# Performance work log

Hardware: AMD Instinct MI355X
Metric: run time of the kernel (lower is better)

Reference implementation:

```python
import jax, jax.numpy as jnp
import numpy as np

# ---- problem dims (match init_kwargs / input_specs) ----
MC = 2048        # max_concepts
D = 128          # embed_dim
B = 64           # batch
L = 16           # program length
NOBJ = 128       # objects per scene
FDIM = 512       # feature_dim
NN = MC + NOBJ   # num_nodes
TEMP = 3.0       # cosine temperature
TH = 0.8         # true_th (cosine, train==val)
POS = 10.0
NEG = -10.0
YES_IDX = 0      # protocol['concepts','yes']
NO_IDX = 1       # protocol['concepts','no']
INIT_VAR = 0.001


def setup_inputs() -> dict:
    key = jax.random.key(0)
    ks = jax.random.split(key, 6)
    scene = jax.random.normal(ks[0], (B, NOBJ, FDIM), jnp.float32)
    # program[:, :, 0] = op code in [0,7), program[:, :, 1] = argument index
    program = jax.random.randint(ks[1], (B, L, 2), 0, 7, dtype=jnp.int32)
    concept_table = jax.random.normal(ks[2], (MC, D), jnp.float32) * INIT_VAR
    relation_table = jax.random.normal(ks[3], (MC, D * D), jnp.float32) * INIT_VAR
    W_feat = jax.random.normal(ks[4], (FDIM, D), jnp.float32) * INIT_VAR
    b_feat = jax.random.normal(ks[5], (D,), jnp.float32) * INIT_VAR
    return {"scene": scene, "program": program, "concept_table": concept_table,
            "relation_table": relation_table, "W_feat": W_feat, "b_feat": b_feat}


def _cos_sim(x, y, eps=1e-8):
    # torch F.cosine_similarity semantics: clamp each norm at eps
    xn = jnp.maximum(jnp.linalg.norm(x, axis=-1), eps)
    yn = jnp.maximum(jnp.linalg.norm(y, axis=-1), eps)
    return jnp.sum(x * y, axis=-1) / (xn * yn)


def reference(scene, program, concept_table, relation_table, W_feat, b_feat):
    # feature_mlp (dim_hidden == 0 -> single Linear)
    objects = scene @ W_feat + b_feat                              # [B, NOBJ, D]
    # per-step embedded arguments
    concept_args = concept_table[program[:, :, 1]]                 # [B, L, D]
    rel_args = relation_table[program[:, :, 1]].reshape(B, L, D, D)
    node_is_concept = jnp.arange(NN) < MC                          # [NN]
    # all_nodes = concat(all_concepts, objects) per sample
    all_nodes = jnp.concatenate(
        [jnp.broadcast_to(concept_table[None], (B, MC, D)), objects], axis=1)  # [B, NN, D]

    def run_sample(nodes_i, ops_i, args_i, cargs_i, rargs_i):
        att0 = jnp.ones((NN,), jnp.float32)

        def body(att, inp):
            op, arg, cvec, rmat = inp

            def f_null(a):
                return a

            def f_sel_obj(a):  # select 'object_only': zero concept slots
                return jnp.where(node_is_concept, 0.0, a)

            def f_sel_con(a):  # select 'concept_only': zero object slots
                return jnp.where(node_is_concept, a, 0.0)

            def f_verify(a):
                sim = _cos_sim(nodes_i, cvec[None, :])             # [NN]
                return jnp.minimum(a, jax.nn.sigmoid((sim - TH) * TEMP))

            def f_choose(a):
                a = jnp.where(node_is_concept, 0.0, a)
                return a.at[arg].set(1.0)

            def f_exist(a):
                s = a.max()
                yes = s * POS
                no = POS - yes
                a = jnp.full_like(a, NEG)
                return a.at[YES_IDX].set(yes).at[NO_IDX].set(no)

            def f_transfer(a):
                gather = a @ nodes_i                               # [D]
                trans = gather @ rmat                              # [D]
                sim = _cos_sim(nodes_i, trans[None, :])            # [NN]
                return jax.nn.sigmoid((sim - TH) * TEMP) * a.max()

            new = jax.lax.switch(
                op, [f_null, f_sel_obj, f_sel_con, f_verify, f_choose,
                     f_exist, f_transfer], att)
            return new, new

        _, hist = jax.lax.scan(body, att0, (ops_i, args_i, cargs_i, rargs_i))
        return hist                                                # [L, NN]

    hist = jax.vmap(run_sample)(all_nodes, program[:, :, 0], program[:, :, 1],
                                concept_args, rel_args)            # [B, L, NN]
    attn_final = hist[:, -1, :MC]                                  # [B, MC]
    out = jax.nn.log_softmax(attn_final, axis=1)
    return out, hist
```

## Files before the change

kernel.cpp:

```cpp
#include <hip/hip_runtime.h>
#include <math.h>

#define MC   2048
#define DD   128
#define BB   64
#define LL   16
#define NOBJ 128
#define FDIM 512
#define NN   (MC + NOBJ)
#define TEMPC 3.0f
#define THC   0.8f
#define POSC  10.0f
#define NEGC  (-10.0f)
#define EPSC  1e-8f
#define NARG  8
#define NINF  (-3.402823466e38f)
#define NSCALE 256.0f

#define QB   4
#define PART (NN / QB)
#define TS   512

typedef unsigned short ushort_t;
typedef float v2f __attribute__((ext_vector_type(2)));

#if defined(__has_builtin)
#if __has_builtin(__builtin_amdgcn_cvt_pk_f32_fp8)
#define HAS_HW_FP8 1
#endif
#endif

__device__ __forceinline__ float e4m3_dec1(unsigned int bv) {
    unsigned int s = (bv >> 7) & 1u, E = (bv >> 3) & 15u, M = bv & 7u;
    float v;
    if (E) v = __uint_as_float(((E + 120u) << 23) | (M << 20));
    else   v = (float)M * 0.001953125f;
    return s ? -v : v;
}
__device__ __forceinline__ v2f f8pair_sw(unsigned int w) {
    v2f r; r[0] = e4m3_dec1(w & 0xffu); r[1] = e4m3_dec1((w >> 8) & 0xffu); return r;
}
#ifdef HAS_HW_FP8
#define F8LO(u) __builtin_amdgcn_cvt_pk_f32_fp8((u), false)
#define F8HI(u) __builtin_amdgcn_cvt_pk_f32_fp8((u), true)
#else
#define F8LO(u) f8pair_sw((u) & 0xffffu)
#define F8HI(u) f8pair_sw((u) >> 16)
#endif

__device__ __forceinline__ unsigned int f32_to_e4m3(float x) {
    float a = fabsf(x);
    unsigned int s = (__float_as_uint(x) >> 31) << 7;
    if (a == 0.0f) return s;
    if (a >= 448.0f) return s | 0x7Eu;
    int e; float m = frexpf(a, &e);
    if (e >= -5) {
        int mant = (int)rintf(m * 16.0f);
        if (mant == 16) { mant = 8; e++; if (e - 1 > 8) return s | 0x7Eu; }
        return s | ((unsigned)(e - 1 + 7) << 3) | (unsigned)(mant - 8);
    } else {
        int q = (int)rintf(a * 512.0f);
        if (q >= 8) return s | 0x08u;
        return s | (unsigned)q;
    }
}

#define DEC16(u, g) do { \
    v2f _p0 = F8LO((u).x), _p1 = F8HI((u).x), _p2 = F8LO((u).y), _p3 = F8HI((u).y); \
    v2f _p4 = F8LO((u).z), _p5 = F8HI((u).z), _p6 = F8LO((u).w), _p7 = F8HI((u).w); \
    g[0]=_p0[0]; g[1]=_p0[1]; g[2]=_p1[0];  g[3]=_p1[1]; \
    g[4]=_p2[0]; g[5]=_p2[1]; g[6]=_p3[0];  g[7]=_p3[1]; \
    g[8]=_p4[0]; g[9]=_p4[1]; g[10]=_p5[0]; g[11]=_p5[1]; \
    g[12]=_p6[0]; g[13]=_p6[1]; g[14]=_p7[0]; g[15]=_p7[1]; \
} while (0)

__global__ __launch_bounds__(256) void gemm_objects(
        const float* __restrict__ scene, const float* __restrict__ W,
        const float* __restrict__ bias, float* __restrict__ obj) {
    __shared__ float sA[64][68];
    __shared__ float sB[64][68];
    const int b  = blockIdx.y;
    const int mt = (blockIdx.x >> 1) * 64;
    const int nt = (blockIdx.x & 1) * 64;
    const int tid = threadIdx.x;
    const int tx = tid & 15, ty = tid >> 4;
    float acc[4][4] = {{0.f,0.f,0.f,0.f},{0.f,0.f,0.f,0.f},{0.f,0.f,0.f,0.f},{0.f,0.f,0.f,0.f}};
    const float* sc = scene + (size_t)b * NOBJ * FDIM;
    for (int k0 = 0; k0 < FDIM; k0 += 64) {
        {
            const int o  = tid >> 2;
            const int ks = (tid & 3) * 16;
            const float4* src = (const float4*)(sc + (size_t)(mt + o) * FDIM + k0 + ks);
            #pragma unroll
            for (int j4 = 0; j4 < 4; j4++) {
                float4 v = src[j4];
                sA[ks + j4*4 + 0][o] = v.x;
                sA[ks + j4*4 + 1][o] = v.y;
                sA[ks + j4*4 + 2][o] = v.z;
                sA[ks + j4*4 + 3][o] = v.w;
            }
        }
        {
            const int kk = tid >> 2;
            const int dq = (tid & 3) * 16;
            const float4* src = (const float4*)(W + (size_t)(k0 + kk) * DD + nt + dq);
            float4* dst = (float4*)&sB[kk][dq];
            #pragma unroll
            for (int j4 = 0; j4 < 4; j4++) dst[j4] = src[j4];
        }
        __syncthreads();
        #pragma unroll 8
        for (int kk = 0; kk < 64; kk++) {
            float4 a4 = *(const float4*)&sA[kk][ty * 4];
            float4 b4 = *(const float4*)&sB[kk][tx * 4];
            float av[4] = {a4.x, a4.y, a4.z, a4.w};
            float bv[4] = {b4.x, b4.y, b4.z, b4.w};
            #pragma unroll
            for (int i = 0; i < 4; i++)
                #pragma unroll
                for (int j = 0; j < 4; j++)
                    acc[i][j] = fmaf(av[i], bv[j], acc[i][j]);
        }
        __syncthreads();
    }
    #pragma unroll
    for (int i = 0; i < 4; i++) {
        const int o = mt + ty * 4 + i;
        float4 r;
        r.x = acc[i][0] + bias[nt + tx*4 + 0];
        r.y = acc[i][1] + bias[nt + tx*4 + 1];
        r.z = acc[i][2] + bias[nt + tx*4 + 2];
        r.w = acc[i][3] + bias[nt + tx*4 + 3];
        *(float4*)(obj + ((size_t)b * NOBJ + o) * DD + nt + tx*4) = r;
    }
}

__global__ __launch_bounds__(256) void norms_prep(
        const float* __restrict__ ct, const float* __restrict__ obj,
        float* __restrict__ cnorm, float* __restrict__ onorm,
        unsigned char* __restrict__ ctf8, unsigned char* __restrict__ objf8,
        unsigned int* __restrict__ ctr) {
    if (blockIdx.x == 0) {
        for (int i = threadIdx.x; i < BB * 16; i += 256) ctr[i] = 0u;
    }
    const int wid = threadIdx.x >> 6, lane = threadIdx.x & 63;
    const int r = blockIdx.x * 4 + wid;
    const int NROWS = MC + BB * NOBJ;
    if (r >= NROWS) return;
    const float* row = (r < MC) ? (ct + (size_t)r * DD) : (obj + (size_t)(r - MC) * DD);
    unsigned char* brow = (r < MC) ? (ctf8 + (size_t)r * DD) : (objf8 + (size_t)(r - MC) * DD);
    float2 xy = *(const float2*)(row + lane * 2);
    float ss = xy.x * xy.x + xy.y * xy.y;
    #pragma unroll
    for (int off = 32; off; off >>= 1) ss += __shfl_xor(ss, off, 64);
    float nrm = fmaxf(sqrtf(ss), EPSC);
    float inv = NSCALE / nrm;
    unsigned int b0 = f32_to_e4m3(xy.x * inv);
    unsigned int b1 = f32_to_e4m3(xy.y * inv);
    *(ushort_t*)(brow + lane * 2) = (ushort_t)(b0 | (b1 << 8));
    if (lane == 0) {
        if (r < MC) cnorm[r] = nrm;
        else        onorm[r - MC] = nrm;
    }
}

__global__ __launch_bounds__(256) void sig_table(
        const float* __restrict__ ct, const float* __restrict__ obj,
        const float* __restrict__ cnorm, const float* __restrict__ onorm,
        float* __restrict__ sigc, float* __restrict__ sigo) {
    __shared__ float cv[NARG][DD];
    __shared__ float cn[NARG];
    const int tid = threadIdx.x;
    for (int a = 0; a < NARG; a++)
        for (int i = tid; i < DD; i += 256) cv[a][i] = ct[(size_t)a * DD + i];
    if (tid < NARG) cn[tid] = fmaxf(cnorm[tid], EPSC);
    __syncthreads();
    const int sub = tid & 7, slot = tid >> 3;
    #pragma unroll
    for (int p = 0; p < 2; p++) {
        const int r = blockIdx.x * 64 + p * 32 + slot;
        const float* row = (r < MC) ? (ct + (size_t)r * DD) : (obj + (size_t)(r - MC) * DD);
        float4 r0 = *(const float4*)(row + sub * 16 + 0);
        float4 r1 = *(const float4*)(row + sub * 16 + 4);
        float4 r2 = *(const float4*)(row + sub * 16 + 8);
        float4 r3 = *(const float4*)(row + sub * 16 + 12);
        float rn = fmaxf((r < MC) ? cnorm[r] : onorm[r - MC], EPSC);
        for (int a = 0; a < NARG; a++) {
            const float* c = &cv[a][sub * 16];
            float dp = 0.f;
            dp = fmaf(r0.x, c[0], dp);  dp = fmaf(r0.y, c[1], dp);
            dp = fmaf(r0.z, c[2], dp);  dp = fmaf(r0.w, c[3], dp);
            dp = fmaf(r1.x, c[4], dp);  dp = fmaf(r1.y, c[5], dp);
            dp = fmaf(r1.z, c[6], dp);  dp = fmaf(r1.w, c[7], dp);
            dp = fmaf(r2.x, c[8], dp);  dp = fmaf(r2.y, c[9], dp);
            dp = fmaf(r2.z, c[10], dp); dp = fmaf(r2.w, c[11], dp);
            dp = fmaf(r3.x, c[12], dp); dp = fmaf(r3.y, c[13], dp);
            dp = fmaf(r3.z, c[14], dp); dp = fmaf(r3.w, c[15], dp);
            dp += __shfl_xor(dp, 1, 64);
            dp += __shfl_xor(dp, 2, 64);
            dp += __shfl_xor(dp, 4, 64);
            if (sub == 0) {
                float sim = dp / (rn * cn[a]);
                float g = 1.f / (1.f + __expf(-(sim - THC) * TEMPC));
                if (r < MC) sigc[(size_t)a * MC + r] = g;
                else {
                    int ro = r - MC, bb = ro >> 7, oo = ro & 127;
                    sigo[((size_t)bb * NARG + a) * NOBJ + oo] = g;
                }
            }
        }
    }
}


#define GATH_ROW(row_) do { \
    const int _r = (row_); \
    uint4 _u = *(const uint4*)&nd[_r * DD + ((sub ^ (_r & 7)) << 4)]; \
    const float _a = att[_r] * nrmL[_r]; \
    float _g[16]; DEC16(_u, _g); \
    _Pragma("unroll") \
    for (int _j = 0; _j < 16; _j++) ac[_j] = fmaf(_a, _g[_j], ac[_j]); \
} while (0)

#define SIM_ROW(row_, COMB) do { \
    const int _r = (row_); \
    uint4 _u = *(const uint4*)&nd[_r * DD + ((sub ^ (_r & 7)) << 4)]; \
    float _g[16]; DEC16(_u, _g); \
    float _dp = 0.f; \
    _Pragma("unroll") \
    for (int _j = 0; _j < 16; _j++) _dp = fmaf(_g[_j], vv[_j], _dp); \
    _dp += __shfl_xor(_dp, 1, 64); \
    _dp += __shfl_xor(_dp, 2, 64); \
    _dp += __shfl_xor(_dp, 4, 64); \
    if (sub == 0) { \
        const float _sim = _dp * invden; \
        const float sg = 1.f / (1.f + __expf(-(_sim - THC) * TEMPC)); \
        COMB; \
    } \
} while (0)

#define QBARRIER() do { \
    __syncthreads(); \
    if (tid == 0) { \
        __threadfence(); \
        __hip_atomic_fetch_add(myctr, 1u, __ATOMIC_RELEASE, __HIP_MEMORY_SCOPE_AGENT); \
        const unsigned _tgt = (unsigned)(QB * epoch); \
        while (__hip_atomic_load(myctr, __ATOMIC_ACQUIRE, __HIP_MEMORY_SCOPE_AGENT) < _tgt) {} \
    } \
    __syncthreads(); \
} while (0)

__global__ __launch_bounds__(TS) void scan_exec(
        const float* __restrict__ ct, const float* __restrict__ rt,
        const int* __restrict__ program,
        const float* __restrict__ cnorm, const float* __restrict__ onorm,
        const float* __restrict__ sigc, const float* __restrict__ sigo,
        const unsigned char* __restrict__ ctf8, const unsigned char* __restrict__ objf8,
        float* __restrict__ gpart, unsigned int* __restrict__ ctr,
        float* __restrict__ out, float* __restrict__ hist) {

    const int b    = blockIdx.x & (BB - 1);
    const int q    = blockIdx.x >> 6;
    const int base = q * PART;
    const int tid  = threadIdx.x;
    const int lane = tid & 63, wid = tid >> 6;
    const int rg   = tid >> 3, sub = tid & 7;

    __shared__ __align__(16) unsigned char nd[PART * DD];
    __shared__ __align__(16) float att[PART];
    __shared__ __align__(16) float nrmL[PART];
    __shared__ __align__(16) float vec[DD];
    __shared__ __align__(16) float gvf[DD];
    __shared__ __align__(16) float part[8 * DD];
    __shared__ float wred[8];
    __shared__ float red2[8];
    __shared__ float s_sh;
    __shared__ int   sprog[2 * LL];

    const unsigned char* myobjf8 = objf8 + (size_t)b * NOBJ * DD;

    for (int idx = tid; idx < PART * 8; idx += TS) {
        const int row = idx >> 3, j = idx & 7;
        const int g   = base + row;
        const unsigned char* src = (g < MC) ? (ctf8 + (size_t)g * DD)
                                            : (myobjf8 + (size_t)(g - MC) * DD);
        uint4 v = *(const uint4*)(src + j * 16);
        *(uint4*)&nd[row * DD + ((j ^ (row & 7)) << 4)] = v;
    }
    for (int i = tid; i < PART; i += TS) {
        const int g = base + i;
        att[i]  = 1.0f;
        nrmL[i] = (g < MC) ? cnorm[g] : onorm[b * NOBJ + (g - MC)];
    }
    if (tid < 2 * LL) sprog[tid] = program[b * 2 * LL + tid];
    __syncthreads();

    unsigned int epoch = 0;
    float* gpb = gpart + (size_t)b * (2 * QB * 132);
    unsigned int* myctr = ctr + b * 16;

    for (int step = 0; step < LL; step++) {
        const int op  = sprog[2 * step];
        const int arg = sprog[2 * step + 1];
        float* hrow = hist + ((size_t)b * LL + step) * NN;

        if (op == 0) {
            for (int i = tid; i < PART; i += TS) hrow[base + i] = att[i];
        } else if (op == 1) {
            for (int i = tid; i < PART; i += TS) {
                const int g = base + i;
                const float nv = (g < MC) ? 0.0f : att[i];
                att[i] = nv; hrow[g] = nv;
            }
        } else if (op == 2) {
            for (int i = tid; i < PART; i += TS) {
                const int g = base + i;
                const float nv = (g < MC) ? att[i] : 0.0f;
                att[i] = nv; hrow[g] = nv;
            }
        } else if (op == 3 && arg < NARG) {
            const float* sc = sigc + (size_t)arg * MC;
            const float* so = sigo + ((size_t)b * NARG + arg) * NOBJ;
            for (int i = tid; i < PART; i += TS) {
                const int g = base + i;
                const float gg = (g < MC) ? sc[g] : so[g - MC];
                const float nv = fminf(att[i], gg);
                att[i] = nv; hrow[g] = nv;
            }
        } else if (op == 3) {
            __syncthreads();
            if (tid < DD) vec[tid] = ct[(size_t)arg * DD + tid];
            __syncthreads();
            const float cn = fmaxf(cnorm[arg], EPSC);
            const float invden = 1.0f / (NSCALE * cn);
            float vv[16];
            {
                const float4 v0 = *(const float4*)&vec[sub * 16 + 0];
                const float4 v1 = *(const float4*)&vec[sub * 16 + 4];
                const float4 v2 = *(const float4*)&vec[sub * 16 + 8];
                const float4 v3 = *(const float4*)&vec[sub * 16 + 12];
                vv[0]=v0.x; vv[1]=v0.y; vv[2]=v0.z; vv[3]=v0.w;
                vv[4]=v1.x; vv[5]=v1.y; vv[6]=v1.z; vv[7]=v1.w;
                vv[8]=v2.x; vv[9]=v2.y; vv[10]=v2.z; vv[11]=v2.w;
                vv[12]=v3.x; vv[13]=v3.y; vv[14]=v3.z; vv[15]=v3.w;
            }
            #pragma unroll
            for (int p = 0; p < 8; p++) SIM_ROW(rg + p * 64, att[_r] = fminf(att[_r], sg));
            if (rg < PART - 512) SIM_ROW(rg + 512, att[_r] = fminf(att[_r], sg));
            __syncthreads();
            for (int i = tid; i < PART; i += TS) hrow[base + i] = att[i];
        } else if (op == 4) {
            for (int i = tid; i < PART; i += TS) {
                const int g = base + i;
                const float nv = (g < MC) ? ((g == arg) ? 1.0f : 0.0f) : att[i];
                att[i] = nv; hrow[g] = nv;
            }
        } else if (op == 5) {
            __syncthreads();
            float lm = NINF;
            for (int i = tid; i < PART; i += TS) lm = fmaxf(lm, att[i]);
            #pragma unroll
            for (int off = 32; off; off >>= 1) lm = fmaxf(lm, __shfl_xor(lm, off, 64));
            if (lane == 0) wred[wid] = lm;
            __syncthreads();
            epoch++;
            if (tid == 0) {
                float m = wred[0];
                #pragma unroll
                for (int w = 1; w < 8; w++) m = fmaxf(m, wred[w]);
                __hip_atomic_store(&gpb[(size_t)((epoch & 1) * QB + q) * 132 + DD], m,
                                   __ATOMIC_RELAXED, __HIP_MEMORY_SCOPE_AGENT);
            }
            QBARRIER();
            if (tid == 0) {
                float* slotR = gpb + (size_t)((epoch & 1) * QB) * 132;
                float m = NINF;
                #pragma unroll
                for (int k = 0; k < QB; k++)
                    m = fmaxf(m, __hip_atomic_load(&slotR[k * 132 + DD],
                                 __ATOMIC_RELAXED, __HIP_MEMORY_SCOPE_AGENT));
                s_sh = m;
            }
            __syncthreads();
            const float s = s_sh;
            const float yes = s * POSC, no = POSC - yes;
            for (int i = tid; i < PART; i += TS) {
                const int g = base + i;
                const float nv = (g == 0) ? yes : ((g == 1) ? no : NEGC);
                att[i] = nv; hrow[g] = nv;
            }
        } else if (op == 6) {
            __syncthreads();
            float lm = NINF;
            for (int i = tid; i < PART; i += TS) lm = fmaxf(lm, att[i]);
            #pragma unroll
            for (int off = 32; off; off >>= 1) lm = fmaxf(lm, __shfl_xor(lm, off, 64));
            if (lane == 0) wred[wid] = lm;
            float ac[16];
            #pragma unroll
            for (int j = 0; j < 16; j++) ac[j] = 0.f;
            #pragma unroll
            for (int p = 0; p < 8; p++) GATH_ROW(rg + p * 64);
            if (rg < PART - 512) GATH_ROW(rg + 512);
            #pragma unroll
            for (int j = 0; j < 16; j++) {
                ac[j] += __shfl_xor(ac[j], 8, 64);
                ac[j] += __shfl_xor(ac[j], 16, 64);
                ac[j] += __shfl_xor(ac[j], 32, 64);
            }
            if (lane < 8) {
                float* dst = &part[wid * DD + lane * 16];
                #pragma unroll
                for (int k = 0; k < 4; k++)
                    *(float4*)(dst + k * 4) = make_float4(ac[k*4], ac[k*4+1], ac[k*4+2], ac[k*4+3]);
            }
            __syncthreads();
            epoch++;
            {
                float* slotW = gpb + (size_t)((epoch & 1) * QB + q) * 132;
                if (tid < DD) {
                    float gsum = 0.f;
                    #pragma unroll
                    for (int w = 0; w < 8; w++) gsum += part[w * DD + tid];
                    __hip_atomic_store(&slotW[tid], gsum, __ATOMIC_RELAXED, __HIP_MEMORY_SCOPE_AGENT);
                }
                if (tid == DD) {
                    float m = wred[0];
                    #pragma unroll
                    for (int w = 1; w < 8; w++) m = fmaxf(m, wred[w]);
                    __hip_atomic_store(&slotW[DD], m, __ATOMIC_RELAXED, __HIP_MEMORY_SCOPE_AGENT);
                }
            }
            const float* rm = rt + (size_t)arg * (DD * DD);
            const int half = lane >> 5, dq = (lane & 31) * 4;
            float4 rmr[8];
            #pragma unroll
            for (int j = 0; j < 8; j++) {
                const int d = wid * 16 + half * 8 + j;
                rmr[j] = *(const float4*)(rm + (size_t)d * DD + dq);
            }
            QBARRIER();
            {
                float* slotR = gpb + (size_t)((epoch & 1) * QB) * 132;
                if (tid < DD) {
                    float gsum = 0.f;
                    #pragma unroll
                    for (int k = 0; k < QB; k++)
                        gsum += __hip_atomic_load(&slotR[k * 132 + tid],
                                  __ATOMIC_RELAXED, __HIP_MEMORY_SCOPE_AGENT);
                    gvf[tid] = gsum;
                }
                if (tid == DD) {
                    float m = NINF;
                    #pragma unroll
                    for (int k = 0; k < QB; k++)
                        m = fmaxf(m, __hip_atomic_load(&slotR[k * 132 + DD],
                                     __ATOMIC_RELAXED, __HIP_MEMORY_SCOPE_AGENT));
                    s_sh = m;
                }
            }
            __syncthreads();
            float qx = 0.f, qy = 0.f, qz = 0.f, qw = 0.f;
            #pragma unroll
            for (int j = 0; j < 8; j++) {
                const int d = wid * 16 + half * 8 + j;
                const float g = gvf[d];
                qx = fmaf(g, rmr[j].x, qx); qy = fmaf(g, rmr[j].y, qy);
                qz = fmaf(g, rmr[j].z, qz); qw = fmaf(g, rmr[j].w, qw);
            }
            qx += __shfl_xor(qx, 32, 64); qy += __shfl_xor(qy, 32, 64);
            qz += __shfl_xor(qz, 32, 64); qw += __shfl_xor(qw, 32, 64);
            if (lane < 32) *(float4*)&part[wid * DD + dq] = make_float4(qx, qy, qz, qw);
            __syncthreads();
            if (tid < DD) {
                float t = 0.f;
                #pragma unroll
                for (int w = 0; w < 8; w++) t += part[w * DD + tid];
                vec[tid] = t;
                float ss = t * t;
                #pragma unroll
                for (int off = 32; off; off >>= 1) ss += __shfl_xor(ss, off, 64);
                if (lane == 0) red2[wid] = ss;
            }
            __syncthreads();
            const float tn = fmaxf(sqrtf(red2[0] + red2[1]), EPSC * NSCALE);
            const float invden = 1.0f / (NSCALE * tn);
            const float s = s_sh;
            float vv[16];
            {
                const float4 v0 = *(const float4*)&vec[sub * 16 + 0];
                const float4 v1 = *(const float4*)&vec[sub * 16 + 4];
                const float4 v2 = *(const float4*)&vec[sub * 16 + 8];
                const float4 v3 = *(const float4*)&vec[sub * 16 + 12];
                vv[0]=v0.x; vv[1]=v0.y; vv[2]=v0.z; vv[3]=v0.w;
                vv[4]=v1.x; vv[5]=v1.y; vv[6]=v1.z; vv[7]=v1.w;
                vv[8]=v2.x; vv[9]=v2.y; vv[10]=v2.z; vv[11]=v2.w;
                vv[12]=v3.x; vv[13]=v3.y; vv[14]=v3.z; vv[15]=v3.w;
            }
            #pragma unroll
            for (int p = 0; p < 8; p++) SIM_ROW(rg + p * 64, att[_r] = sg * s);
            if (rg < PART - 512) SIM_ROW(rg + 512, att[_r] = sg * s);
            __syncthreads();
            for (int i = tid; i < PART; i += TS) hrow[base + i] = att[i];
        }
    }

    __syncthreads();
    const int crows = (base + PART <= MC) ? PART : (MC - base);
    {
        float lm = NINF;
        for (int i = tid; i < crows; i += TS) lm = fmaxf(lm, att[i]);
        #pragma unroll
        for (int off = 32; off; off >>= 1) lm = fmaxf(lm, __shfl_xor(lm, off, 64));
        if (lane == 0) wred[wid] = lm;
    }
    __syncthreads();
    epoch++;
    if (tid == 0) {
        float m = wred[0];
        #pragma unroll
        for (int w = 1; w < 8; w++) m = fmaxf(m, wred[w]);
        __hip_atomic_store(&gpb[(size_t)((epoch & 1) * QB + q) * 132 + DD], m,
                           __ATOMIC_RELAXED, __HIP_MEMORY_SCOPE_AGENT);
    }
    QBARRIER();
    if (tid == 0) {
        float* slotR = gpb + (size_t)((epoch & 1) * QB) * 132;
        float m = NINF;
        #pragma unroll
        for (int k = 0; k < QB; k++)
            m = fmaxf(m, __hip_atomic_load(&slotR[k * 132 + DD],
                         __ATOMIC_RELAXED, __HIP_MEMORY_SCOPE_AGENT));
        s_sh = m;
    }
    __syncthreads();
    const float mglob = s_sh;
    {
        float lse = 0.f;
        for (int i = tid; i < crows; i += TS) lse += expf(att[i] - mglob);
        #pragma unroll
        for (int off = 32; off; off >>= 1) lse += __shfl_xor(lse, off, 64);
        if (lane == 0) wred[wid] = lse;
    }
    __syncthreads();
    epoch++;
    if (tid == 0) {
        float se = 0.f;
        #pragma unroll
        for (int w = 0; w < 8; w++) se += wred[w];
        __hip_atomic_store(&gpb[(size_t)((epoch & 1) * QB + q) * 132 + DD], se,
                           __ATOMIC_RELAXED, __HIP_MEMORY_SCOPE_AGENT);
    }
    QBARRIER();
    if (tid == 0) {
        float* slotR = gpb + (size_t)((epoch & 1) * QB) * 132;
        float se = 0.f;
        #pragma unroll
        for (int k = 0; k < QB; k++)
            se += __hip_atomic_load(&slotR[k * 132 + DD],
                    __ATOMIC_RELAXED, __HIP_MEMORY_SCOPE_AGENT);
        s_sh = se;
    }
    __syncthreads();
    const float ls = logf(s_sh);
    for (int i = tid; i < crows; i += TS)
        out[(size_t)b * MC + base + i] = att[i] - mglob - ls;
}

extern "C" void kernel_launch(void* const* d_in, const int* in_sizes, int n_in,
                              void* d_out, int out_size, void* d_ws, size_t ws_size,
                              hipStream_t stream) {
    const float* scene = (const float*)d_in[0];
    const int*   prog  = (const int*)d_in[1];
    const float* ct    = (const float*)d_in[2];
    const float* rt    = (const float*)d_in[3];
    const float* W     = (const float*)d_in[4];
    const float* bias  = (const float*)d_in[5];

    float* out  = (float*)d_out;
    float* hist = out + (size_t)BB * MC;

    float* obj   = (float*)d_ws;
    float* cnorm = obj + (size_t)BB * NOBJ * DD;
    float* onorm = cnorm + MC;
    float* sigc  = onorm + (size_t)BB * NOBJ;
    float* sigo  = sigc + (size_t)NARG * MC;
    float* gpart = sigo + (size_t)BB * NARG * NOBJ;
    unsigned int* ctrbuf = (unsigned int*)(gpart + (size_t)BB * 2 * QB * 132);
    unsigned char* ctf8  = (unsigned char*)(ctrbuf + BB * 16);
    unsigned char* objf8 = ctf8 + (size_t)MC * DD;

    gemm_objects<<<dim3(4, BB), 256, 0, stream>>>(scene, W, bias, obj);
    norms_prep<<<dim3((MC + BB * NOBJ) / 4), 256, 0, stream>>>(ct, obj, cnorm, onorm,
                                                               ctf8, objf8, ctrbuf);
    sig_table<<<dim3((MC + BB * NOBJ) / 64), 256, 0, stream>>>(ct, obj, cnorm, onorm, sigc, sigo);
    scan_exec<<<dim3(BB * QB), TS, 0, stream>>>(ct, rt, prog, cnorm, onorm, sigc, sigo,
                                                ctf8, objf8, gpart, ctrbuf, out, hist);
}
```

Measured before the change: 320.6 us.

## Fuse prep kernels, relax barrier ordering, merge log-softmax reductions into one barrier

Merges norms_prep and sig_table into one launch, with the sig blocks recomputing norms locally so they no longer depend on the other kernel's output. The cross-block barrier drops its threadfence and acquire/release ordering in favour of relaxed atomics plus s_sleep polling. The final log-softmax uses a local max and sum combined online across blocks, removing one global barrier. The relation-matrix register load is hoisted ahead of the reductions to overlap its latency. The relaxed ordering risks memory visibility errors across blocks, and the norms are now computed twice.

Result: faster. 259.5 us (-19.0%).

```diff
diff --git a/kernel.cpp b/kernel.cpp
--- a/kernel.cpp
+++ b/kernel.cpp
@@ -135,56 +135,71 @@
     }
 }
 
-__global__ __launch_bounds__(256) void norms_prep(
+#define NBN ((MC + BB * NOBJ) / 4)
+
+__global__ __launch_bounds__(256) void prep_fused(
         const float* __restrict__ ct, const float* __restrict__ obj,
         float* __restrict__ cnorm, float* __restrict__ onorm,
         unsigned char* __restrict__ ctf8, unsigned char* __restrict__ objf8,
-        unsigned int* __restrict__ ctr) {
-    if (blockIdx.x == 0) {
-        for (int i = threadIdx.x; i < BB * 16; i += 256) ctr[i] = 0u;
-    }
-    const int wid = threadIdx.x >> 6, lane = threadIdx.x & 63;
-    const int r = blockIdx.x * 4 + wid;
-    const int NROWS = MC + BB * NOBJ;
-    if (r >= NROWS) return;
-    const float* row = (r < MC) ? (ct + (size_t)r * DD) : (obj + (size_t)(r - MC) * DD);
-    unsigned char* brow = (r < MC) ? (ctf8 + (size_t)r * DD) : (objf8 + (size_t)(r - MC) * DD);
-    float2 xy = *(const float2*)(row + lane * 2);
-    float ss = xy.x * xy.x + xy.y * xy.y;
-    #pragma unroll
-    for (int off = 32; off; off >>= 1) ss += __shfl_xor(ss, off, 64);
-    float nrm = fmaxf(sqrtf(ss), EPSC);
-    float inv = NSCALE / nrm;
-    unsigned int b0 = f32_to_e4m3(xy.x * inv);
-    unsigned int b1 = f32_to_e4m3(xy.y * inv);
-    *(ushort_t*)(brow + lane * 2) = (ushort_t)(b0 | (b1 << 8));
-    if (lane == 0) {
-        if (r < MC) cnorm[r] = nrm;
-        else        onorm[r - MC] = nrm;
-    }
-}
-
-__global__ __launch_bounds__(256) void sig_table(
-        const float* __restrict__ ct, const float* __restrict__ obj,
-        const float* __restrict__ cnorm, const float* __restrict__ onorm,
+        unsigned int* __restrict__ ctr,
         float* __restrict__ sigc, float* __restrict__ sigo) {
+    if (blockIdx.x < NBN) {
+        if (blockIdx.x == 0) {
+            for (int i = threadIdx.x; i < BB * 16; i += 256) ctr[i] = 0u;
+        }
+        const int wid = threadIdx.x >> 6, lane = threadIdx.x & 63;
+        const int r = blockIdx.x * 4 + wid;
+        const float* row = (r < MC) ? (ct + (size_t)r * DD) : (obj + (size_t)(r - MC) * DD);
+        unsigned char* brow = (r < MC) ? (ctf8 + (size_t)r * DD) : (objf8 + (size_t)(r - MC) * DD);
+        float2 xy = *(const float2*)(row + lane * 2);
+        float ss = xy.x * xy.x + xy.y * xy.y;
+        #pragma unroll
+        for (int off = 32; off; off >>= 1) ss += __shfl_xor(ss, off, 64);
+        float nrm = fmaxf(sqrtf(ss), EPSC);
+        float inv = NSCALE / nrm;
+        unsigned int b0 = f32_to_e4m3(xy.x * inv);
+        unsigned int b1 = f32_to_e4m3(xy.y * inv);
+        *(ushort_t*)(brow + lane * 2) = (ushort_t)(b0 | (b1 << 8));
+        if (lane == 0) {
+            if (r < MC) cnorm[r] = nrm;
+            else        onorm[r - MC] = nrm;
+        }
+        return;
+    }
     __shared__ float cv[NARG][DD];
     __shared__ float cn[NARG];
     const int tid = threadIdx.x;
     for (int a = 0; a < NARG; a++)
         for (int i = tid; i < DD; i += 256) cv[a][i] = ct[(size_t)a * DD + i];
-    if (tid < NARG) cn[tid] = fmaxf(cnorm[tid], EPSC);
+    __syncthreads();
+    if (tid < NARG) {
+        float ss = 0.f;
+        for (int i = 0; i < DD; i++) ss = fmaf(cv[tid][i], cv[tid][i], ss);
+        cn[tid] = fmaxf(sqrtf(ss), EPSC);
+    }
     __syncthreads();
     const int sub = tid & 7, slot = tid >> 3;
     #pragma unroll
     for (int p = 0; p < 2; p++) {
-        const int r = blockIdx.x * 64 + p * 32 + slot;
+        const int r = (blockIdx.x - NBN) * 64 + p * 32 + slot;
         const float* row = (r < MC) ? (ct + (size_t)r * DD) : (obj + (size_t)(r - MC) * DD);
         float4 r0 = *(const float4*)(row + sub * 16 + 0);
         float4 r1 = *(const float4*)(row + sub * 16 + 4);
         float4 r2 = *(const float4*)(row + sub * 16 + 8);
         float4 r3 = *(const float4*)(row + sub * 16 + 12);
-        float rn = fmaxf((r < MC) ? cnorm[r] : onorm[r - MC], EPSC);
+        float ssr = 0.f;
+        ssr = fmaf(r0.x, r0.x, ssr); ssr = fmaf(r0.y, r0.y, ssr);
+        ssr = fmaf(r0.z, r0.z, ssr); ssr = fmaf(r0.w, r0.w, ssr);
+        ssr = fmaf(r1.x, r1.x, ssr); ssr = fmaf(r1.y, r1.y, ssr);
+        ssr = fmaf(r1.z, r1.z, ssr); ssr = fmaf(r1.w, r1.w, ssr);
+        ssr = fmaf(r2.x, r2.x, ssr); ssr = fmaf(r2.y, r2.y, ssr);
+        ssr = fmaf(r2.z, r2.z, ssr); ssr = fmaf(r2.w, r2.w, ssr);
+        ssr = fmaf(r3.x, r3.x, ssr); ssr = fmaf(r3.y, r3.y, ssr);
+        ssr = fmaf(r3.z, r3.z, ssr); ssr = fmaf(r3.w, r3.w, ssr);
+        ssr += __shfl_xor(ssr, 1, 64);
+        ssr += __shfl_xor(ssr, 2, 64);
+        ssr += __shfl_xor(ssr, 4, 64);
+        float rn = fmaxf(sqrtf(ssr), EPSC);
         for (int a = 0; a < NARG; a++) {
             const float* c = &cv[a][sub * 16];
             float dp = 0.f;
@@ -239,13 +254,16 @@
     } \
 } while (0)
 
+#define AST(p, v) __hip_atomic_store((p), (v), __ATOMIC_RELAXED, __HIP_MEMORY_SCOPE_AGENT)
+#define ALD(p)    __hip_atomic_load((p), __ATOMIC_RELAXED, __HIP_MEMORY_SCOPE_AGENT)
+
 #define QBARRIER() do { \
     __syncthreads(); \
     if (tid == 0) { \
-        __threadfence(); \
-        __hip_atomic_fetch_add(myctr, 1u, __ATOMIC_RELEASE, __HIP_MEMORY_SCOPE_AGENT); \
+        __hip_atomic_fetch_add(myctr, 1u, __ATOMIC_RELAXED, __HIP_MEMORY_SCOPE_AGENT); \
         const unsigned _tgt = (unsigned)(QB * epoch); \
-        while (__hip_atomic_load(myctr, __ATOMIC_ACQUIRE, __HIP_MEMORY_SCOPE_AGENT) < _tgt) {} \
+        while (__hip_atomic_load(myctr, __ATOMIC_RELAXED, __HIP_MEMORY_SCOPE_AGENT) < _tgt) \
+            __builtin_amdgcn_s_sleep(1); \
     } \
     __syncthreads(); \
 } while (0)
@@ -271,10 +289,11 @@
     __shared__ __align__(16) float nrmL[PART];
     __shared__ __align__(16) float vec[DD];
     __shared__ __align__(16) float gvf[DD];
-    __shared__ __align__(16) float part[8 * DD];
+    __shared__ __align__(16) float part[14 * DD];
     __shared__ float wred[8];
     __shared__ float red2[8];
     __shared__ float s_sh;
+    __shared__ float s_sh2;
     __shared__ int   sprog[2 * LL];
 
     const unsigned char* myobjf8 = objf8 + (size_t)b * NOBJ * DD;
@@ -368,8 +387,7 @@
                 float m = wred[0];
                 #pragma unroll
                 for (int w = 1; w < 8; w++) m = fmaxf(m, wred[w]);
-                __hip_atomic_store(&gpb[(size_t)((epoch & 1) * QB + q) * 132 + DD], m,
-                                   __ATOMIC_RELAXED, __HIP_MEMORY_SCOPE_AGENT);
+                AST(&gpb[(size_t)((epoch & 1) * QB + q) * 132 + DD], m);
             }
             QBARRIER();
             if (tid == 0) {
@@ -377,8 +395,7 @@
                 float m = NINF;
                 #pragma unroll
                 for (int k = 0; k < QB; k++)
-                    m = fmaxf(m, __hip_atomic_load(&slotR[k * 132 + DD],
-                                 __ATOMIC_RELAXED, __HIP_MEMORY_SCOPE_AGENT));
+                    m = fmaxf(m, ALD(&slotR[k * 132 + DD]));
                 s_sh = m;
             }
             __syncthreads();
@@ -391,6 +408,14 @@
             }
         } else if (op == 6) {
             __syncthreads();
+            const float* rm = rt + (size_t)arg * (DD * DD);
+            const int half = lane >> 5, dq = (lane & 31) * 4;
+            float4 rmr[8];
+            #pragma unroll
+            for (int j = 0; j < 8; j++) {
+                const int d = wid * 16 + half * 8 + j;
+                rmr[j] = *(const float4*)(rm + (size_t)d * DD + dq);
+            }
             float lm = NINF;
             for (int i = tid; i < PART; i += TS) lm = fmaxf(lm, att[i]);
             #pragma unroll
@@ -422,22 +447,14 @@
                     float gsum = 0.f;
                     #pragma unroll
                     for (int w = 0; w < 8; w++) gsum += part[w * DD + tid];
-                    __hip_atomic_store(&slotW[tid], gsum, __ATOMIC_RELAXED, __HIP_MEMORY_SCOPE_AGENT);
+                    AST(&slotW[tid], gsum);
                 }
                 if (tid == DD) {
                     float m = wred[0];
                     #pragma unroll
                     for (int w = 1; w < 8; w++) m = fmaxf(m, wred[w]);
-                    __hip_atomic_store(&slotW[DD], m, __ATOMIC_RELAXED, __HIP_MEMORY_SCOPE_AGENT);
+                    AST(&slotW[DD], m);
                 }
-            }
-            const float* rm = rt + (size_t)arg * (DD * DD);
-            const int half = lane >> 5, dq = (lane & 31) * 4;
-            float4 rmr[8];
-            #pragma unroll
-            for (int j = 0; j < 8; j++) {
-                const int d = wid * 16 + half * 8 + j;
-                rmr[j] = *(const float4*)(rm + (size_t)d * DD + dq);
             }
             QBARRIER();
             {
@@ -446,16 +463,14 @@
                     float gsum = 0.f;
                     #pragma unroll
                     for (int k = 0; k < QB; k++)
-                        gsum += __hip_atomic_load(&slotR[k * 132 + tid],
-                                  __ATOMIC_RELAXED, __HIP_MEMORY_SCOPE_AGENT);
+                        gsum += ALD(&slotR[k * 132 + tid]);
                     gvf[tid] = gsum;
                 }
                 if (tid == DD) {
                     float m = NINF;
                     #pragma unroll
                     for (int k = 0; k < QB; k++)
-                        m = fmaxf(m, __hip_atomic_load(&slotR[k * 132 + DD],
-                                     __ATOMIC_RELAXED, __HIP_MEMORY_SCOPE_AGENT));
+                        m = fmaxf(m, ALD(&slotR[k * 132 + DD]));
                     s_sh = m;
                 }
             }
@@ -515,54 +530,45 @@
         if (lane == 0) wred[wid] = lm;
     }
     __syncthreads();
+    float mloc = wred[0];
+    #pragma unroll
+    for (int w = 1; w < 8; w++) mloc = fmaxf(mloc, wred[w]);
+    {
+        float lse = 0.f;
+        for (int i = tid; i < crows; i += TS) lse += expf(att[i] - mloc);
+        #pragma unroll
+        for (int off = 32; off; off >>= 1) lse += __shfl_xor(lse, off, 64);
+        if (lane == 0) red2[wid] = lse;
+    }
+    __syncthreads();
     epoch++;
     if (tid == 0) {
-        float m = wred[0];
+        float sloc = 0.f;
         #pragma unroll
-        for (int w = 1; w < 8; w++) m = fmaxf(m, wred[w]);
-        __hip_atomic_store(&gpb[(size_t)((epoch & 1) * QB + q) * 132 + DD], m,
-                           __ATOMIC_RELAXED, __HIP_MEMORY_SCOPE_AGENT);
+        for (int w = 0; w < 8; w++) sloc += red2[w];
+        float* slotW = gpb + (size_t)((epoch & 1) * QB + q) * 132;
+        AST(&slotW[DD], mloc);
+        AST(&slotW[DD + 1], sloc);
     }
     QBARRIER();
     if (tid == 0) {
         float* slotR = gpb + (size_t)((epoch & 1) * QB) * 132;
-        float m = NINF;
+        float mg = NINF;
+        float mq[QB], sq[QB];
         #pragma unroll
-        for (int k = 0; k < QB; k++)
-            m = fmaxf(m, __hip_atomic_load(&slotR[k * 132 + DD],
-                         __ATOMIC_RELAXED, __HIP_MEMORY_SCOPE_AGENT));
-        s_sh = m;
-    }
-    __syncthreads();
-    const float mglob = s_sh;
-    {
-        float lse = 0.f;
-        for (int i = tid; i < crows; i += TS) lse += expf(att[i] - mglob);
-        #pragma unroll
-        for (int off = 32; off; off >>= 1) lse += __shfl_xor(lse, off, 64);
-        if (lane == 0) wred[wid] = lse;
-    }
-    __syncthreads();
-    epoch++;
-    if (tid == 0) {
+        for (int k = 0; k < QB; k++) {
+            mq[k] = ALD(&slotR[k * 132 + DD]);
+            sq[k] = ALD(&slotR[k * 132 + DD + 1]);
+            mg = fmaxf(mg, mq[k]);
+        }
         float se = 0.f;
         #pragma unroll
-        for (int w = 0; w < 8; w++) se += wred[w];
-        __hip_atomic_store(&gpb[(size_t)((epoch & 1) * QB + q) * 132 + DD], se,
-                           __ATOMIC_RELAXED, __HIP_MEMORY_SCOPE_AGENT);
-    }
-    QBARRIER();
-    if (tid == 0) {
-        float* slotR = gpb + (size_t)((epoch & 1) * QB) * 132;
-        float se = 0.f;
-        #pragma unroll
-        for (int k = 0; k < QB; k++)
-            se += __hip_atomic_load(&slotR[k * 132 + DD],
-                    __ATOMIC_RELAXED, __HIP_MEMORY_SCOPE_AGENT);
-        s_sh = se;
+        for (int k = 0; k < QB; k++) se += sq[k] * expf(mq[k] - mg);
+        s_sh  = mg;
+        s_sh2 = logf(se);
     }
     __syncthreads();
-    const float ls = logf(s_sh);
+    const float mglob = s_sh, ls = s_sh2;
     for (int i = tid; i < crows; i += TS)
         out[(size_t)b * MC + base + i] = att[i] - mglob - ls;
 }
@@ -591,9 +597,8 @@
     unsigned char* objf8 = ctf8 + (size_t)MC * DD;
 
     gemm_objects<<<dim3(4, BB), 256, 0, stream>>>(scene, W, bias, obj);
-    norms_prep<<<dim3((MC + BB * NOBJ) / 4), 256, 0, stream>>>(ct, obj, cnorm, onorm,
-                                                               ctf8, objf8, ctrbuf);
-    sig_table<<<dim3((MC + BB * NOBJ) / 64), 256, 0, stream>>>(ct, obj, cnorm, onorm, sigc, sigo);
+    prep_fused<<<dim3(NBN + (MC + BB * NOBJ) / 64), 256, 0, stream>>>(
+        ct, obj, cnorm, onorm, ctf8, objf8, ctrbuf, sigc, sigo);
     scan_exec<<<dim3(BB * QB), TS, 0, stream>>>(ct, rt, prog, cnorm, onorm, sigc, sigo,
                                                 ctf8, objf8, gpart, ctrbuf, out, hist);
 }
```
